# Performance work log

Hardware: AMD Instinct MI355X
Metric: run time of the kernel (lower is better)

## Reference

```python
import jax, jax.numpy as jnp
import numpy as np

I_T = 0.5      # IoU threshold
EPS = 1e-07    # FocalLoss eps
GAMMA = 2.0    # FocalLoss gamma
C_IN = 500
N_CLS = 3


def _box_iou(boxes):
    # boxes: (P, 4) in xyxy -> pairwise IoU (P, P), matching torchvision.ops.box_iou
    area = (boxes[:, 2] - boxes[:, 0]) * (boxes[:, 3] - boxes[:, 1])
    lt = jnp.maximum(boxes[:, None, :2], boxes[None, :, :2])
    rb = jnp.minimum(boxes[:, None, 2:], boxes[None, :, 2:])
    wh = jnp.clip(rb - lt, 0.0)
    inter = wh[..., 0] * wh[..., 1]
    return inter / (area[:, None] + area[None, :] - inter)


def setup_inputs() -> dict:
    key = jax.random.key(0)
    k1, k2, k3, k4, k5, k6, k7 = jax.random.split(key, 7)
    bs, P = 16, 2048
    inputs = jax.random.normal(k1, (bs * P, C_IN), jnp.float32)
    pre_score = jax.random.uniform(k2, (bs, P, N_CLS), jnp.float32)
    labels = jax.random.randint(k3, (bs, N_CLS), 0, 2).astype(bool)
    # valid xyxy boxes in a ~512x512 image
    xy1 = jax.random.uniform(k4, (bs, P, 2), jnp.float32) * 400.0
    wh = jax.random.uniform(k5, (bs, P, 2), jnp.float32) * 104.0 + 8.0
    rois = jnp.concatenate([xy1, xy1 + wh], axis=-1)
    fc_w = jax.random.normal(k6, (4, C_IN), jnp.float32) * (1.0 / np.sqrt(C_IN))
    fc_b = jax.random.normal(k7, (4,), jnp.float32) * 0.01
    return {"inputs": inputs, "pre_score": pre_score, "labels": labels,
            "rois": rois, "num": 2048, "fc_w": fc_w, "fc_b": fc_b}


def reference(inputs, pre_score, labels, rois, num, fc_w, fc_b):
    bs = pre_score.shape[0]
    P = num
    dt = inputs.dtype

    # fc + softmax over class dim
    xr_k = jax.nn.softmax((inputs @ fc_w.T + fc_b).reshape(bs, P, 4), axis=2)

    # pairwise IoU per batch: (bs, P, P)
    iou = jax.vmap(_box_iou)(rois)

    # candidate seed proposals: score > 0.5; fallback to single argmax when <= 1 candidate
    cand = pre_score > 0.5                                   # (bs, P, 3)
    ncand = cand.sum(axis=1, keepdims=True)                  # (bs, 1, 3)
    fb = jax.nn.one_hot(jnp.argmax(pre_score, axis=1), P, axis=1, dtype=bool)  # (bs, P, 3)
    cand = jnp.where(ncand <= 1, fb, cand)
    lab = labels.astype(bool)

    # sequential (c = 0,1,2) strict-greater argmax assignment, as in the torch loops
    I = jnp.zeros((bs, P), dt)
    w = jnp.zeros((bs, P), dt)
    hits = []
    for c in range(N_CLS):
        m = jnp.where(cand[:, None, :, c], iou, -1.0)        # mask non-candidate columns
        best = m.max(axis=-1)                                # (bs, P)
        jstar = m.argmax(axis=-1)                            # first-max tie-break, as torch
        xbest = jnp.take_along_axis(pre_score[:, :, c], jstar, axis=1)
        best = jnp.where(lab[:, c:c + 1], best, -1.0)        # class skipped if label off
        upd = best > I
        w = jnp.where(upd, xbest, w)
        hits.append(upd & (best > I_T))
        I = jnp.where(upd, best, I)
    h = jnp.stack(hits, axis=-1)                             # (bs, P, 3)
    y_k = jnp.concatenate([h.astype(dt),
                           (~h.any(axis=-1, keepdims=True)).astype(dt)], axis=-1)
    target = jnp.argmax(y_k.reshape(bs * P, 4), axis=1)      # first class with y==1, else 3

    # FocalLoss(gamma=2) applied to already-softmaxed scores (double softmax, as original)
    logit = jnp.clip(jax.nn.softmax(xr_k.reshape(bs * P, 4), axis=1), EPS, 1.0 - EPS)
    pt = jnp.take_along_axis(logit, target[:, None], axis=1)[:, 0]
    floss = -jnp.log(pt) * (1.0 - pt) ** GAMMA               # (N,)

    # original computes mean(w.view(N,1) * loss(N,)) which broadcasts to (N,N);
    # that equals mean(w) * mean(loss) -- computed without materializing N^2.
    loss = jnp.mean(w.reshape(-1)) * jnp.mean(floss)
    return (xr_k, loss)
```

## Files before the change

kernel.cpp:

```cpp
#include <hip/hip_runtime.h>
#include <math.h>

#define BS   16
#define PP   2048
#define CIN  500
#define NROW (BS * PP)
#define JQ   256
#define NQ   8
#define IT   256
#define NIT  8
#define NBLK_IOU (BS * NIT * NQ)
#define NBT2 128
#define HIMASK 0xFFFFF800u

typedef int v8i __attribute__((ext_vector_type(8)));

__global__ void __launch_bounds__(256) prep_kernel(
    const float* __restrict__ pre_score, const float* __restrict__ rois,
    uint4* __restrict__ rec2)
{
    int b = blockIdx.x;
    int tid = threadIdx.x;
    __shared__ float sv[256];
    __shared__ int   si[256];
    __shared__ int   sc[256];

    float v0[8], v1[8], v2[8];
    unsigned char bits[8];
#pragma unroll
    for (int t = 0; t < 8; ++t) {
        int j = t * 256 + tid;
        const float* p = pre_score + ((size_t)b * PP + j) * 3;
        v0[t] = p[0]; v1[t] = p[1]; v2[t] = p[2];
        bits[t] = 0;
    }

#define PREP_CLASS(VV, CBIT)                                                   \
    {                                                                          \
        float bv = -1.0f; int bi = 0; int cnt = 0;                             \
        _Pragma("unroll")                                                      \
        for (int t = 0; t < 8; ++t) {                                          \
            int j = t * 256 + tid;                                             \
            float v = VV[t];                                                   \
            if (v > 0.5f) cnt++;                                               \
            if (v > bv) { bv = v; bi = j; }                                    \
        }                                                                      \
        sv[tid] = bv; si[tid] = bi; sc[tid] = cnt;                             \
        __syncthreads();                                                       \
        for (int s2 = 128; s2 > 0; s2 >>= 1) {                                 \
            if (tid < s2) {                                                    \
                float ov = sv[tid + s2]; int oi = si[tid + s2];                \
                if (ov > sv[tid] || (ov == sv[tid] && oi < si[tid])) {         \
                    sv[tid] = ov; si[tid] = oi;                                \
                }                                                              \
                sc[tid] += sc[tid + s2];                                       \
            }                                                                  \
            __syncthreads();                                                   \
        }                                                                      \
        int total = sc[0];                                                     \
        int amax  = si[0];                                                     \
        __syncthreads();                                                       \
        _Pragma("unroll")                                                      \
        for (int t = 0; t < 8; ++t) {                                          \
            int j = t * 256 + tid;                                             \
            bool cb = (total <= 1) ? (j == amax) : (VV[t] > 0.5f);             \
            if (cb) bits[t] |= (unsigned char)(CBIT);                          \
        }                                                                      \
    }

    PREP_CLASS(v0, 1)
    PREP_CLASS(v1, 2)
    PREP_CLASS(v2, 4)
#undef PREP_CLASS

    const float4* rb = (const float4*)(rois + (size_t)b * PP * 4);
#pragma unroll
    for (int t = 0; t < 8; ++t) {
        int j = t * 256 + tid;
        float4 bx = rb[j];
        float area = (bx.z - bx.x) * (bx.w - bx.y);
        uint4 lo, hi;
        lo.x = __float_as_uint(bx.x);
        lo.y = __float_as_uint(bx.y);
        lo.z = __float_as_uint(bx.z);
        lo.w = __float_as_uint(bx.w);
        hi.x = __float_as_uint(area);
        hi.y = (bits[t] & 1) ? 0xFFFFFFFFu : 0u;
        hi.z = (bits[t] & 2) ? 0xFFFFFFFFu : 0u;
        hi.w = (bits[t] & 4) ? 0xFFFFFFFFu : 0u;
        rec2[((size_t)b * PP + j) * 2 + 0] = lo;
        rec2[((size_t)b * PP + j) * 2 + 1] = hi;
    }
}

__global__ void __launch_bounds__(512, 4) fused_kernel(
    const float* __restrict__ rois, const unsigned* __restrict__ rec2d,
    unsigned* __restrict__ qres,
    const float* __restrict__ inputs, const float* __restrict__ fc_w,
    const float* __restrict__ fc_b, float* __restrict__ out)
{
    __shared__ unsigned bestA[3][8][IT];
    int bid = blockIdx.x;
    int q   = bid & 7;
    int it  = (bid >> 3) & 7;
    int b   = bid >> 6;
    int tid = threadIdx.x, lane = tid & 63;
    int w   = __builtin_amdgcn_readfirstlane(tid >> 6);

    float4 wr[4][2];
#pragma unroll
    for (int c = 0; c < 4; ++c) {
        const float4* wrow = (const float4*)(fc_w + c * CIN);
        wr[c][0] = wrow[lane];
        wr[c][1] = (lane < 61) ? wrow[64 + lane]
                               : make_float4(0.f, 0.f, 0.f, 0.f);
    }
    int row0 = bid * 32 + w * 4;
    int f1 = (lane < 61) ? 64 + lane : 0;
    float4 xin[4][2];
#pragma unroll
    for (int r = 0; r < 4; ++r) {
        const float4* in4 = (const float4*)(inputs + (size_t)(row0 + r) * CIN);
        xin[r][0] = in4[lane];
        xin[r][1] = in4[f1];
    }

    const float4* rbase = (const float4*)(rois + (size_t)b * PP * 4);
    float4 bx[4];
    float  ax[4];
#pragma unroll
    for (int s = 0; s < 4; ++s) {
        bx[s] = rbase[it * IT + s * 64 + lane];
        ax[s] = (bx[s].z - bx[s].x) * (bx[s].w - bx[s].y);
    }

    int jb  = q * JQ + w * 32;
    int jfb = 2047 - jb;
    unsigned long long addr = (unsigned long long)rec2d
                            + (unsigned long long)(b * PP + jb) * 32ull;

    unsigned best[4][3];
#pragma unroll
    for (int s = 0; s < 4; ++s) { best[s][0] = 0u; best[s][1] = 0u; best[s][2] = 0u; }

    v8i A0, A1, A2, A3, B0, B1, B2, B3;

#define ISSUE4(R0, R1, R2, R3)                                                 \
    asm volatile("s_load_dwordx8 %0, %1, 0x0"  : "=&s"(R0) : "s"(addr));       \
    asm volatile("s_load_dwordx8 %0, %1, 0x20" : "=&s"(R1) : "s"(addr));       \
    asm volatile("s_load_dwordx8 %0, %1, 0x40" : "=&s"(R2) : "s"(addr));       \
    asm volatile("s_load_dwordx8 %0, %1, 0x60" : "=&s"(R3) : "s"(addr));       \
    addr += 128;

#define DO_J(R, KOFF)                                                          \
    {                                                                          \
        float bjx = __uint_as_float((unsigned)R[0]);                           \
        float bjy = __uint_as_float((unsigned)R[1]);                           \
        float bjz = __uint_as_float((unsigned)R[2]);                           \
        float bjw = __uint_as_float((unsigned)R[3]);                           \
        float aj  = __uint_as_float((unsigned)R[4]);                           \
        unsigned m0 = (unsigned)R[5], m1 = (unsigned)R[6], m2 = (unsigned)R[7];\
        unsigned jf = (unsigned)(jfb - (KOFF));                                \
        _Pragma("unroll")                                                      \
        for (int s = 0; s < 4; ++s) {                                          \
            float lx = fmaxf(bx[s].x, bjx), ly = fmaxf(bx[s].y, bjy);          \
            float rx = fminf(bx[s].z, bjz), ry = fminf(bx[s].w, bjw);          \
            float ww = fmaxf(rx - lx, 0.f), hh = fmaxf(ry - ly, 0.f);          \
            float inter = ww * hh;                                             \
            float uni   = (ax[s] + aj) - inter;                                \
            float iou   = inter * __builtin_amdgcn_rcpf(uni);                  \
            unsigned pk = (__float_as_uint(iou) & HIMASK) | jf;                \
            unsigned k0 = pk & m0, k1 = pk & m1, k2 = pk & m2;                 \
            best[s][0] = best[s][0] > k0 ? best[s][0] : k0;                    \
            best[s][1] = best[s][1] > k1 ? best[s][1] : k1;                    \
            best[s][2] = best[s][2] > k2 ? best[s][2] : k2;                    \
        }                                                                      \
    }

#define BATCH(C0, C1, C2, C3, N0, N1, N2, N3, BASE, DOISSUE)                   \
    asm volatile("s_waitcnt lgkmcnt(0)"                                        \
                 : "+s"(C0), "+s"(C1), "+s"(C2), "+s"(C3));                    \
    __builtin_amdgcn_sched_barrier(0);                                         \
    if (DOISSUE) { ISSUE4(N0, N1, N2, N3) }                                    \
    DO_J(C0, (BASE) + 0) DO_J(C1, (BASE) + 1)                                  \
    DO_J(C2, (BASE) + 2) DO_J(C3, (BASE) + 3)

    ISSUE4(A0, A1, A2, A3)
    BATCH(A0, A1, A2, A3, B0, B1, B2, B3,  0, 1)
    BATCH(B0, B1, B2, B3, A0, A1, A2, A3,  4, 1)
    BATCH(A0, A1, A2, A3, B0, B1, B2, B3,  8, 1)
    BATCH(B0, B1, B2, B3, A0, A1, A2, A3, 12, 1)
    BATCH(A0, A1, A2, A3, B0, B1, B2, B3, 16, 1)
    BATCH(B0, B1, B2, B3, A0, A1, A2, A3, 20, 1)
    BATCH(A0, A1, A2, A3, B0, B1, B2, B3, 24, 1)
    BATCH(B0, B1, B2, B3, A0, A1, A2, A3, 28, 0)

#undef BATCH
#undef DO_J
#undef ISSUE4

#pragma unroll
    for (int s = 0; s < 4; ++s) {
        bestA[0][w][s * 64 + lane] = best[s][0];
        bestA[1][w][s * 64 + lane] = best[s][1];
        bestA[2][w][s * 64 + lane] = best[s][2];
    }
    __syncthreads();

    if (tid < IT) {
#pragma unroll
        for (int c = 0; c < 3; ++c) {
            unsigned m = bestA[c][0][tid];
#pragma unroll
            for (int w2 = 1; w2 < 8; ++w2) {
                unsigned o = bestA[c][w2][tid];
                m = m > o ? m : o;
            }
            qres[(((size_t)b * NQ + q) * 3 + c) * PP + it * IT + tid] = m;
        }
    }

#pragma unroll
    for (int r = 0; r < 4; ++r) {
        float a0 = 0.f, a1 = 0.f, a2 = 0.f, a3 = 0.f;
#pragma unroll
        for (int t = 0; t < 2; ++t) {
            float4 x = xin[r][t];
            a0 += x.x * wr[0][t].x + x.y * wr[0][t].y + x.z * wr[0][t].z + x.w * wr[0][t].w;
            a1 += x.x * wr[1][t].x + x.y * wr[1][t].y + x.z * wr[1][t].z + x.w * wr[1][t].w;
            a2 += x.x * wr[2][t].x + x.y * wr[2][t].y + x.z * wr[2][t].z + x.w * wr[2][t].w;
            a3 += x.x * wr[3][t].x + x.y * wr[3][t].y + x.z * wr[3][t].z + x.w * wr[3][t].w;
        }
#pragma unroll
        for (int off = 32; off > 0; off >>= 1) {
            a0 += __shfl_xor(a0, off);
            a1 += __shfl_xor(a1, off);
            a2 += __shfl_xor(a2, off);
            a3 += __shfl_xor(a3, off);
        }
        if (lane == 0) {
            a0 += fc_b[0]; a1 += fc_b[1]; a2 += fc_b[2]; a3 += fc_b[3];
            float m = fmaxf(fmaxf(a0, a1), fmaxf(a2, a3));
            float e0 = expf(a0 - m), e1 = expf(a1 - m);
            float e2 = expf(a2 - m), e3 = expf(a3 - m);
            float inv = 1.0f / (e0 + e1 + e2 + e3);
            ((float4*)out)[row0 + r] = make_float4(e0 * inv, e1 * inv, e2 * inv, e3 * inv);
        }
    }
}

__global__ void __launch_bounds__(256) merge_focal_kernel(
    const unsigned* __restrict__ qres, const float* __restrict__ pre_score,
    const int* __restrict__ labels, const float* __restrict__ xr,
    float* __restrict__ partials)
{
    __shared__ float redw[4], redf[4];
    int bt = blockIdx.x;
    int b = bt >> 3, it = bt & 7;
    int tid = threadIdx.x;
    int i = it * IT + tid;

    float I = 0.f, wv = 0.f;
    int target = 3;
#pragma unroll
    for (int c = 0; c < 3; ++c) {
        unsigned k = 0u;
#pragma unroll
        for (int qq = 0; qq < NQ; ++qq) {
            unsigned h = qres[(((size_t)b * NQ + qq) * 3 + c) * PP + i];
            k = k > h ? k : h;
        }
        int   jv    = 2047 - (int)(k & 2047u);
        float bestv = __uint_as_float(k & HIMASK);
        bestv = (labels[b * 3 + c] != 0) ? bestv : -1.0f;
        if (bestv > I) {
            wv = pre_score[((size_t)b * PP + jv) * 3 + c];
            if (bestv > 0.5f && target == 3) target = c;
            I = bestv;
        }
    }
    int gi = b * PP + i;
    float4 x4 = ((const float4*)xr)[gi];
    float m = fmaxf(fmaxf(x4.x, x4.y), fmaxf(x4.z, x4.w));
    float e0 = expf(x4.x - m), e1 = expf(x4.y - m), e2 = expf(x4.z - m), e3 = expf(x4.w - m);
    float ssum = e0 + e1 + e2 + e3;
    float et = (target == 0) ? e0 : (target == 1) ? e1 : (target == 2) ? e2 : e3;
    float pt = et / ssum;
    pt = fminf(fmaxf(pt, 1e-7f), 1.0f - 1e-7f);
    float fl = -logf(pt) * (1.0f - pt) * (1.0f - pt);

    float sw = wv, sf = fl;
#pragma unroll
    for (int off = 32; off > 0; off >>= 1) {
        sw += __shfl_down(sw, off);
        sf += __shfl_down(sf, off);
    }
    if ((tid & 63) == 0) { redw[tid >> 6] = sw; redf[tid >> 6] = sf; }
    __syncthreads();
    if (tid == 0) {
        partials[bt * 2 + 0] = redw[0] + redw[1] + redw[2] + redw[3];
        partials[bt * 2 + 1] = redf[0] + redf[1] + redf[2] + redf[3];
    }
}

__global__ void __launch_bounds__(256) finalize_kernel(
    const float* __restrict__ partials, float* __restrict__ out_loss)
{
    __shared__ float swL[256], sfL[256];
    int tid = threadIdx.x;
    float sw = (tid < NBT2) ? partials[2 * tid] : 0.f;
    float sf = (tid < NBT2) ? partials[2 * tid + 1] : 0.f;
    swL[tid] = sw; sfL[tid] = sf;
    __syncthreads();
    for (int s = 128; s > 0; s >>= 1) {
        if (tid < s) { swL[tid] += swL[tid + s]; sfL[tid] += sfL[tid + s]; }
        __syncthreads();
    }
    if (tid == 0)
        out_loss[0] = (swL[0] / (float)NROW) * (sfL[0] / (float)NROW);
}

extern "C" void kernel_launch(void* const* d_in, const int* in_sizes, int n_in,
                              void* d_out, int out_size, void* d_ws, size_t ws_size,
                              hipStream_t stream)
{
    const float* inputs    = (const float*)d_in[0];
    const float* pre_score = (const float*)d_in[1];
    const int*   labels    = (const int*)d_in[2];
    const float* rois      = (const float*)d_in[3];
    const float* fc_w      = (const float*)d_in[5];
    const float* fc_b      = (const float*)d_in[6];

    float* out = (float*)d_out;
    char* ws = (char*)d_ws;
    unsigned* qres     = (unsigned*)ws;
    uint4*    rec2     = (uint4*)(ws + 3145728);
    float*    partials = (float*)(ws + 3145728 + 1048576);

    prep_kernel<<<BS, 256, 0, stream>>>(pre_score, rois, rec2);
    fused_kernel<<<NBLK_IOU, 512, 0, stream>>>(rois, (const unsigned*)rec2, qres,
                                               inputs, fc_w, fc_b, out);
    merge_focal_kernel<<<NBT2, 256, 0, stream>>>(qres, pre_score, labels, out, partials);
    finalize_kernel<<<1, 256, 0, stream>>>(partials, out + (size_t)NROW * 4);
}
```

Before: 63.26 us.

## Sort boxes by x1 and skip non-overlapping IoU tiles via x-range bounds

Adds a per-batch bitonic sort of boxes by x1 and repacks the box records in sorted order, with a permutation array and per-tile x-min/x-max bounds. In the fused IoU kernel each j box is tested against the tile's x range, and the IoU math is skipped when it cannot overlap, cutting the pairwise arithmetic. The candidate computation is split into a per-(batch,class) kernel. The cost is an extra kernel launch, a serial-ish sort in one block per batch, a permutation gather in the merge step, and a divergent branch in the hot loop.

```diff
diff --git a/kernel.cpp b/kernel.cpp
--- a/kernel.cpp
+++ b/kernel.cpp
@@ -15,86 +15,120 @@
 
 typedef int v8i __attribute__((ext_vector_type(8)));
 
-__global__ void __launch_bounds__(256) prep_kernel(
-    const float* __restrict__ pre_score, const float* __restrict__ rois,
-    uint4* __restrict__ rec2)
-{
-    int b = blockIdx.x;
+__global__ void __launch_bounds__(256) cand_kernel(
+    const float* __restrict__ pre_score, unsigned* __restrict__ cmask)
+{
+    int bc = blockIdx.x;
+    int b = bc / 3, c = bc - b * 3;
     int tid = threadIdx.x;
     __shared__ float sv[256];
     __shared__ int   si[256];
-    __shared__ int   sc[256];
-
-    float v0[8], v1[8], v2[8];
-    unsigned char bits[8];
+    __shared__ int   sn[256];
+
+    float v[8];
 #pragma unroll
     for (int t = 0; t < 8; ++t) {
         int j = t * 256 + tid;
-        const float* p = pre_score + ((size_t)b * PP + j) * 3;
-        v0[t] = p[0]; v1[t] = p[1]; v2[t] = p[2];
-        bits[t] = 0;
-    }
-
-#define PREP_CLASS(VV, CBIT)                                                   \
-    {                                                                          \
-        float bv = -1.0f; int bi = 0; int cnt = 0;                             \
-        _Pragma("unroll")                                                      \
-        for (int t = 0; t < 8; ++t) {                                          \
-            int j = t * 256 + tid;                                             \
-            float v = VV[t];                                                   \
-            if (v > 0.5f) cnt++;                                               \
-            if (v > bv) { bv = v; bi = j; }                                    \
-        }                                                                      \
-        sv[tid] = bv; si[tid] = bi; sc[tid] = cnt;                             \
-        __syncthreads();                                                       \
-        for (int s2 = 128; s2 > 0; s2 >>= 1) {                                 \
-            if (tid < s2) {                                                    \
-                float ov = sv[tid + s2]; int oi = si[tid + s2];                \
-                if (ov > sv[tid] || (ov == sv[tid] && oi < si[tid])) {         \
-                    sv[tid] = ov; si[tid] = oi;                                \
-                }                                                              \
-                sc[tid] += sc[tid + s2];                                       \
-            }                                                                  \
-            __syncthreads();                                                   \
-        }                                                                      \
-        int total = sc[0];                                                     \
-        int amax  = si[0];                                                     \
-        __syncthreads();                                                       \
-        _Pragma("unroll")                                                      \
-        for (int t = 0; t < 8; ++t) {                                          \
-            int j = t * 256 + tid;                                             \
-            bool cb = (total <= 1) ? (j == amax) : (VV[t] > 0.5f);             \
-            if (cb) bits[t] |= (unsigned char)(CBIT);                          \
-        }                                                                      \
-    }
-
-    PREP_CLASS(v0, 1)
-    PREP_CLASS(v1, 2)
-    PREP_CLASS(v2, 4)
-#undef PREP_CLASS
-
-    const float4* rb = (const float4*)(rois + (size_t)b * PP * 4);
+        v[t] = pre_score[((size_t)b * PP + j) * 3 + c];
+    }
+    float bv = -1.0f; int bi = 0; int cnt = 0;
 #pragma unroll
     for (int t = 0; t < 8; ++t) {
         int j = t * 256 + tid;
-        float4 bx = rb[j];
+        if (v[t] > 0.5f) cnt++;
+        if (v[t] > bv) { bv = v[t]; bi = j; }
+    }
+    sv[tid] = bv; si[tid] = bi; sn[tid] = cnt;
+    __syncthreads();
+    for (int s2 = 128; s2 > 0; s2 >>= 1) {
+        if (tid < s2) {
+            float ov = sv[tid + s2]; int oi = si[tid + s2];
+            if (ov > sv[tid] || (ov == sv[tid] && oi < si[tid])) { sv[tid] = ov; si[tid] = oi; }
+            sn[tid] += sn[tid + s2];
+        }
+        __syncthreads();
+    }
+    int total = sn[0];
+    int amax  = si[0];
+#pragma unroll
+    for (int t = 0; t < 8; ++t) {
+        int j = t * 256 + tid;
+        bool cb = (total <= 1) ? (j == amax) : (v[t] > 0.5f);
+        cmask[(size_t)bc * PP + j] = cb ? 1u : 0u;
+    }
+}
+
+__global__ void __launch_bounds__(512) sortpack_kernel(
+    const float* __restrict__ rois, const unsigned* __restrict__ cmask,
+    uint4* __restrict__ rec2, int* __restrict__ perm,
+    float2* __restrict__ tileinfo)
+{
+    __shared__ unsigned skey[PP];
+    __shared__ float    sx2[PP];
+    int b = blockIdx.x;
+    int tid = threadIdx.x;
+    const float4* rb = (const float4*)(rois + (size_t)b * PP * 4);
+
+    for (int p = tid; p < PP; p += 512)
+        skey[p] = (__float_as_uint(rb[p].x) & 0xFFFFF800u) | (unsigned)p;
+    __syncthreads();
+
+    for (unsigned k = 2; k <= PP; k <<= 1) {
+        for (unsigned jj = k >> 1; jj > 0; jj >>= 1) {
+            for (int p = tid; p < PP; p += 512) {
+                unsigned ixj = (unsigned)p ^ jj;
+                if (ixj > (unsigned)p) {
+                    unsigned a = skey[p], b2 = skey[ixj];
+                    bool up = ((p & k) == 0);
+                    if ((a > b2) == up) { skey[p] = b2; skey[ixj] = a; }
+                }
+            }
+            __syncthreads();
+        }
+    }
+
+    float tminr = 0.f;
+    if (tid < 8) tminr = __uint_as_float(skey[tid * 256] & 0xFFFFF800u);
+
+    for (int t = 0; t < 4; ++t) {
+        int p = t * 512 + tid;
+        unsigned o = skey[p] & 0x7FFu;
+        float4 bx = rb[o];
+        sx2[p] = bx.z;
         float area = (bx.z - bx.x) * (bx.w - bx.y);
+        unsigned jfm = 0xFFFFF800u | (2047u - o);
+        unsigned c0 = cmask[((size_t)b * 3 + 0) * PP + o];
+        unsigned c1 = cmask[((size_t)b * 3 + 1) * PP + o];
+        unsigned c2 = cmask[((size_t)b * 3 + 2) * PP + o];
         uint4 lo, hi;
         lo.x = __float_as_uint(bx.x);
         lo.y = __float_as_uint(bx.y);
         lo.z = __float_as_uint(bx.z);
         lo.w = __float_as_uint(bx.w);
         hi.x = __float_as_uint(area);
-        hi.y = (bits[t] & 1) ? 0xFFFFFFFFu : 0u;
-        hi.z = (bits[t] & 2) ? 0xFFFFFFFFu : 0u;
-        hi.w = (bits[t] & 4) ? 0xFFFFFFFFu : 0u;
-        rec2[((size_t)b * PP + j) * 2 + 0] = lo;
-        rec2[((size_t)b * PP + j) * 2 + 1] = hi;
-    }
+        hi.y = c0 ? jfm : 0u;
+        hi.z = c1 ? jfm : 0u;
+        hi.w = c2 ? jfm : 0u;
+        rec2[((size_t)b * PP + p) * 2 + 0] = lo;
+        rec2[((size_t)b * PP + p) * 2 + 1] = hi;
+        perm[(size_t)b * PP + p] = (int)o;
+    }
+    __syncthreads();
+    for (int s = 128; s > 0; s >>= 1) {
+        for (int t2 = tid; t2 < 8 * s; t2 += 512) {
+            int seg = t2 / s, off = t2 - seg * s;
+            int base = seg * 256 + off;
+            float a2 = sx2[base], b2 = sx2[base + s];
+            sx2[base] = a2 > b2 ? a2 : b2;
+        }
+        __syncthreads();
+    }
+    if (tid < 8)
+        tileinfo[b * 8 + tid] = make_float2(tminr, sx2[tid * 256]);
 }
 
 __global__ void __launch_bounds__(512, 4) fused_kernel(
-    const float* __restrict__ rois, const unsigned* __restrict__ rec2d,
+    const unsigned* __restrict__ rec2d, const float2* __restrict__ tileinfo,
     unsigned* __restrict__ qres,
     const float* __restrict__ inputs, const float* __restrict__ fc_w,
     const float* __restrict__ fc_b, float* __restrict__ out)
@@ -125,17 +159,21 @@
         xin[r][1] = in4[f1];
     }
 
-    const float4* rbase = (const float4*)(rois + (size_t)b * PP * 4);
+    const uint4* rbase2 = (const uint4*)rec2d + (size_t)b * PP * 2;
     float4 bx[4];
     float  ax[4];
 #pragma unroll
     for (int s = 0; s < 4; ++s) {
-        bx[s] = rbase[it * IT + s * 64 + lane];
+        uint4 lo = rbase2[(size_t)(it * IT + s * 64 + lane) * 2];
+        bx[s] = make_float4(__uint_as_float(lo.x), __uint_as_float(lo.y),
+                            __uint_as_float(lo.z), __uint_as_float(lo.w));
         ax[s] = (bx[s].z - bx[s].x) * (bx[s].w - bx[s].y);
     }
 
-    int jb  = q * JQ + w * 32;
-    int jfb = 2047 - jb;
+    float2 ti = tileinfo[(b << 3) | it];
+    float tmin = ti.x, tmax = ti.y;
+
+    int jb = q * JQ + w * 32;
     unsigned long long addr = (unsigned long long)rec2d
                             + (unsigned long long)(b * PP + jb) * 32ull;
 
@@ -152,48 +190,50 @@
     asm volatile("s_load_dwordx8 %0, %1, 0x60" : "=&s"(R3) : "s"(addr));       \
     addr += 128;
 
-#define DO_J(R, KOFF)                                                          \
+#define DO_J(R)                                                                \
     {                                                                          \
         float bjx = __uint_as_float((unsigned)R[0]);                           \
-        float bjy = __uint_as_float((unsigned)R[1]);                           \
         float bjz = __uint_as_float((unsigned)R[2]);                           \
-        float bjw = __uint_as_float((unsigned)R[3]);                           \
-        float aj  = __uint_as_float((unsigned)R[4]);                           \
-        unsigned m0 = (unsigned)R[5], m1 = (unsigned)R[6], m2 = (unsigned)R[7];\
-        unsigned jf = (unsigned)(jfb - (KOFF));                                \
-        _Pragma("unroll")                                                      \
-        for (int s = 0; s < 4; ++s) {                                          \
-            float lx = fmaxf(bx[s].x, bjx), ly = fmaxf(bx[s].y, bjy);          \
-            float rx = fminf(bx[s].z, bjz), ry = fminf(bx[s].w, bjw);          \
-            float ww = fmaxf(rx - lx, 0.f), hh = fmaxf(ry - ly, 0.f);          \
-            float inter = ww * hh;                                             \
-            float uni   = (ax[s] + aj) - inter;                                \
-            float iou   = inter * __builtin_amdgcn_rcpf(uni);                  \
-            unsigned pk = (__float_as_uint(iou) & HIMASK) | jf;                \
-            unsigned k0 = pk & m0, k1 = pk & m1, k2 = pk & m2;                 \
-            best[s][0] = best[s][0] > k0 ? best[s][0] : k0;                    \
-            best[s][1] = best[s][1] > k1 ? best[s][1] : k1;                    \
-            best[s][2] = best[s][2] > k2 ? best[s][2] : k2;                    \
+        if (!(bjx > tmax || bjz < tmin)) {                                     \
+            float bjy = __uint_as_float((unsigned)R[1]);                       \
+            float bjw = __uint_as_float((unsigned)R[3]);                       \
+            float aj  = __uint_as_float((unsigned)R[4]);                       \
+            unsigned m0 = (unsigned)R[5], m1 = (unsigned)R[6];                 \
+            unsigned m2 = (unsigned)R[7];                                      \
+            unsigned jfx = (m0 | m1 | m2) & 0x7FFu;                            \
+            _Pragma("unroll")                                                  \
+            for (int s = 0; s < 4; ++s) {                                      \
+                float lx = fmaxf(bx[s].x, bjx), ly = fmaxf(bx[s].y, bjy);      \
+                float rx = fminf(bx[s].z, bjz), ry = fminf(bx[s].w, bjw);      \
+                float ww = fmaxf(rx - lx, 0.f), hh = fmaxf(ry - ly, 0.f);      \
+                float inter = ww * hh;                                         \
+                float uni   = (ax[s] + aj) - inter;                            \
+                float iou   = inter * __builtin_amdgcn_rcpf(uni);              \
+                unsigned pk = (__float_as_uint(iou) & HIMASK) | jfx;           \
+                unsigned k0 = pk & m0, k1 = pk & m1, k2 = pk & m2;             \
+                best[s][0] = best[s][0] > k0 ? best[s][0] : k0;                \
+                best[s][1] = best[s][1] > k1 ? best[s][1] : k1;                \
+                best[s][2] = best[s][2] > k2 ? best[s][2] : k2;                \
+            }                                                                  \
         }                                                                      \
     }
 
-#define BATCH(C0, C1, C2, C3, N0, N1, N2, N3, BASE, DOISSUE)                   \
+#define BATCH(C0, C1, C2, C3, N0, N1, N2, N3, DOISSUE)                         \
     asm volatile("s_waitcnt lgkmcnt(0)"                                        \
                  : "+s"(C0), "+s"(C1), "+s"(C2), "+s"(C3));                    \
     __builtin_amdgcn_sched_barrier(0);                                         \
     if (DOISSUE) { ISSUE4(N0, N1, N2, N3) }                                    \
-    DO_J(C0, (BASE) + 0) DO_J(C1, (BASE) + 1)                                  \
-    DO_J(C2, (BASE) + 2) DO_J(C3, (BASE) + 3)
+    DO_J(C0) DO_J(C1) DO_J(C2) DO_J(C3)
 
     ISSUE4(A0, A1, A2, A3)
-    BATCH(A0, A1, A2, A3, B0, B1, B2, B3,  0, 1)
-    BATCH(B0, B1, B2, B3, A0, A1, A2, A3,  4, 1)
-    BATCH(A0, A1, A2, A3, B0, B1, B2, B3,  8, 1)
-    BATCH(B0, B1, B2, B3, A0, A1, A2, A3, 12, 1)
-    BATCH(A0, A1, A2, A3, B0, B1, B2, B3, 16, 1)
-    BATCH(B0, B1, B2, B3, A0, A1, A2, A3, 20, 1)
-    BATCH(A0, A1, A2, A3, B0, B1, B2, B3, 24, 1)
-    BATCH(B0, B1, B2, B3, A0, A1, A2, A3, 28, 0)
+    BATCH(A0, A1, A2, A3, B0, B1, B2, B3, 1)
+    BATCH(B0, B1, B2, B3, A0, A1, A2, A3, 1)
+    BATCH(A0, A1, A2, A3, B0, B1, B2, B3, 1)
+    BATCH(B0, B1, B2, B3, A0, A1, A2, A3, 1)
+    BATCH(A0, A1, A2, A3, B0, B1, B2, B3, 1)
+    BATCH(B0, B1, B2, B3, A0, A1, A2, A3, 1)
+    BATCH(A0, A1, A2, A3, B0, B1, B2, B3, 1)
+    BATCH(B0, B1, B2, B3, A0, A1, A2, A3, 0)
 
 #undef BATCH
 #undef DO_J
@@ -250,9 +290,9 @@
 }
 
 __global__ void __launch_bounds__(256) merge_focal_kernel(
-    const unsigned* __restrict__ qres, const float* __restrict__ pre_score,
-    const int* __restrict__ labels, const float* __restrict__ xr,
-    float* __restrict__ partials)
+    const unsigned* __restrict__ qres, const int* __restrict__ perm,
+    const float* __restrict__ pre_score, const int* __restrict__ labels,
+    const float* __restrict__ xr, float* __restrict__ partials)
 {
     __shared__ float redw[4], redf[4];
     int bt = blockIdx.x;
@@ -279,7 +319,8 @@
             I = bestv;
         }
     }
-    int gi = b * PP + i;
+    int o = perm[(size_t)b * PP + i];
+    int gi = b * PP + o;
     float4 x4 = ((const float4*)xr)[gi];
     float m = fmaxf(fmaxf(x4.x, x4.y), fmaxf(x4.z, x4.w));
     float e0 = expf(x4.x - m), e1 = expf(x4.y - m), e2 = expf(x4.z - m), e3 = expf(x4.w - m);
@@ -335,11 +376,15 @@
     char* ws = (char*)d_ws;
     unsigned* qres     = (unsigned*)ws;
     uint4*    rec2     = (uint4*)(ws + 3145728);
-    float*    partials = (float*)(ws + 3145728 + 1048576);
-
-    prep_kernel<<<BS, 256, 0, stream>>>(pre_score, rois, rec2);
-    fused_kernel<<<NBLK_IOU, 512, 0, stream>>>(rois, (const unsigned*)rec2, qres,
+    unsigned* cmask    = (unsigned*)(ws + 4194304);
+    int*      perm     = (int*)(ws + 4587520);
+    float2*   tileinfo = (float2*)(ws + 4718592);
+    float*    partials = (float*)(ws + 4719616);
+
+    cand_kernel<<<BS * 3, 256, 0, stream>>>(pre_score, cmask);
+    sortpack_kernel<<<BS, 512, 0, stream>>>(rois, cmask, rec2, perm, tileinfo);
+    fused_kernel<<<NBLK_IOU, 512, 0, stream>>>((const unsigned*)rec2, tileinfo, qres,
                                                inputs, fc_w, fc_b, out);
-    merge_focal_kernel<<<NBT2, 256, 0, stream>>>(qres, pre_score, labels, out, partials);
+    merge_focal_kernel<<<NBT2, 256, 0, stream>>>(qres, perm, pre_score, labels, out, partials);
     finalize_kernel<<<1, 256, 0, stream>>>(partials, out + (size_t)NROW * 4);
 }
```

Result: slower. 103.7 us (+63.9%).
